# Performance work log

Hardware: AMD Instinct MI355X
Metric: run time of the kernel (lower is better)

Reference implementation:

```python
import jax, jax.numpy as jnp
import numpy as np

IMG = 100          # IMG_SIZE
NQ = 4             # N_QUBITS
STEP = 2           # sqrt(NQ)
NP_SIDE = IMG // STEP   # 50 patches per side
NPATCH = NP_SIDE * NP_SIDE  # 2500

# Fixed surrogate for tq.RandomLayer(n_ops=8): 6 param rotations + 2 CNOTs
OPS = [("rx", 0), ("ry", 1), ("rz", 2), ("cnot", (0, 1)),
       ("rx", 3), ("cnot", (2, 3)), ("ry", 0), ("rz", 1)]


def _apply_1q(psi, G, w):
    # psi: [N,2,2,2,2] complex, G: [2,2] complex, wire w
    out = jnp.tensordot(G, psi, axes=[[1], [w + 1]])  # new wire axis at 0
    return jnp.moveaxis(out, 0, w + 1)


def _apply_cnot(psi, c, t):
    p0 = jax.lax.index_in_dim(psi, 0, axis=c + 1, keepdims=True)
    p1 = jax.lax.index_in_dim(psi, 1, axis=c + 1, keepdims=True)
    p1 = jnp.flip(p1, axis=t + 1)  # X on target when control=1
    return jnp.concatenate([p0, p1], axis=c + 1)


def _gate(name, t):
    tc = t.astype(jnp.complex64)
    c, s = jnp.cos(tc / 2), jnp.sin(tc / 2)
    if name == "rx":
        return jnp.stack([jnp.stack([c, -1j * s]), jnp.stack([-1j * s, c])])
    if name == "ry":
        return jnp.stack([jnp.stack([c, -s]), jnp.stack([s, c])])
    # rz
    em, ep = jnp.exp(-0.5j * tc), jnp.exp(0.5j * tc)
    z = jnp.zeros_like(em)
    return jnp.stack([jnp.stack([em, z]), jnp.stack([z, ep])])


def _quanv(x, q_params):
    # x: [B,100,100] -> batched 4-qubit statevector sim over all patches
    B = x.shape[0]
    # patch pixel order: [x[c,r], x[c,r+1], x[c+1,r], x[c+1,r+1]]
    p = x.reshape(B, NP_SIDE, STEP, NP_SIDE, STEP)
    p = p.transpose(0, 1, 3, 2, 4).reshape(B * NPATCH, NQ)  # [N,4] angles
    half = 0.5 * p
    a = jnp.stack([jnp.cos(half), jnp.sin(half)], axis=-1)  # [N,4,2] RY|0>
    psi = jnp.einsum("na,nb,nc,nd->nabcd", a[:, 0], a[:, 1], a[:, 2], a[:, 3])
    psi = psi.astype(jnp.complex64)
    pi = 0
    for name, w in OPS:
        if name == "cnot":
            psi = _apply_cnot(psi, w[0], w[1])
        else:
            psi = _apply_1q(psi, _gate(name, q_params[pi]), w)
            pi += 1
    probs = jnp.abs(psi) ** 2  # [N,2,2,2,2] real
    zsign = jnp.array([1.0, -1.0], dtype=probs.dtype)
    exps = []
    for w in range(NQ):
        zb = zsign.reshape((1,) + (1,) * w + (2,) + (1,) * (NQ - 1 - w))
        exps.append((probs * zb).sum(axis=(1, 2, 3, 4)))
    meas = jnp.stack(exps, axis=-1)  # [N,4] PauliZ expvals
    return meas.reshape(B, NPATCH * NQ).astype(jnp.float32)  # [B,10000]


def setup_inputs() -> dict:
    key = jax.random.key(0)
    k1, k2, k3, k4 = jax.random.split(key, 4)
    x = jax.random.uniform(k1, (64, IMG, IMG), dtype=jnp.float32)
    W = jax.random.normal(k2, (2, IMG * IMG), dtype=jnp.float32) * 0.01
    b = jax.random.normal(k3, (2,), dtype=jnp.float32) * 0.01
    q_params = jax.random.uniform(k4, (6,), dtype=jnp.float32) * 2.0 * np.pi
    return {"x": x, "W": W, "b": b, "q_params": q_params}


def reference(x, W, b, q_params):
    feats = jax.lax.stop_gradient(_quanv(x, q_params))  # torch.no_grad() block
    logits = feats @ W.T + b
    return jax.nn.log_softmax(logits, axis=-1)
```

## Files before the change

### kernel.cpp

```cpp
#include <hip/hip_runtime.h>
#include <math.h>

#define IMG      100
#define NPS      50
#define NPATCH   2500
#define NIMG     64
#define BLK      1024


__global__ __launch_bounds__(BLK) void quanv_fused_kernel(
    const float* __restrict__ x,
    const float* __restrict__ W,
    const float* __restrict__ bias,
    const float* __restrict__ qp,
    float* __restrict__ out)
{
    const int b = blockIdx.x;

    const float C0 = __cosf(qp[0]);
    float S1, C1;  __sincosf(qp[1], &S1, &C1);
    const float C3 = __cosf(qp[3]);
    float S4, C4;  __sincosf(qp[4], &S4, &C4);

    const float k_a = C0 * C4;
    const float k_b = S4 * C1;
    const float k_c = S4 * S1;
    const float k_d = C0 * C1;
    const float k_e = C0 * S1;
    const float k_f = C3;

    float t0 = 0.0f, t1 = 0.0f;

    const float* xb = x + b * (IMG * IMG);

    for (int p = threadIdx.x; p < NPATCH; p += BLK) {
        const int pi = p / NPS;
        const int pj = p - pi * NPS;

        const float2 r0 = *reinterpret_cast<const float2*>(xb + (2 * pi) * IMG + 2 * pj);
        const float2 r1 = *reinterpret_cast<const float2*>(xb + (2 * pi + 1) * IMG + 2 * pj);
        const float x0 = r0.x, x1 = r0.y, x2 = r1.x, x3 = r1.y;

        float sx0, cz0, sx1, cz1;
        __sincosf(x0, &sx0, &cz0);
        __sincosf(x1, &sx1, &cz1);
        const float cz2 = __cosf(x2);
        const float cz3 = __cosf(x3);

        const float e0 = k_a * cz0 - k_b * sx0 * sx1 - k_c * sx0 * cz1;
        const float e1 = k_d * cz0 * cz1 - k_e * cz0 * sx1;
        const float e2 = cz2;
        const float e3 = k_f * cz2 * cz3;

        const float4 w0 = reinterpret_cast<const float4*>(W)[p];
        const float4 w1 = reinterpret_cast<const float4*>(W)[NPATCH + p];
        t0 += e0 * w0.x + e1 * w0.y + e2 * w0.z + e3 * w0.w;
        t1 += e0 * w1.x + e1 * w1.y + e2 * w1.z + e3 * w1.w;
    }

    #pragma unroll
    for (int off = 32; off > 0; off >>= 1) {
        t0 += __shfl_down(t0, off);
        t1 += __shfl_down(t1, off);
    }
    __shared__ float red0[BLK / 64], red1[BLK / 64];
    const int lane = threadIdx.x & 63;
    const int wv   = threadIdx.x >> 6;
    if (lane == 0) { red0[wv] = t0; red1[wv] = t1; }
    __syncthreads();
    if (threadIdx.x == 0) {
        float l0 = 0.f, l1 = 0.f;
        #pragma unroll
        for (int w = 0; w < BLK / 64; ++w) { l0 += red0[w]; l1 += red1[w]; }
        l0 += bias[0];
        l1 += bias[1];
        float m   = fmaxf(l0, l1);
        float lse = m + logf(__expf(l0 - m) + __expf(l1 - m));
        out[b * 2 + 0] = l0 - lse;
        out[b * 2 + 1] = l1 - lse;
    }
}

extern "C" void kernel_launch(void* const* d_in, const int* in_sizes, int n_in,
                              void* d_out, int out_size, void* d_ws, size_t ws_size,
                              hipStream_t stream) {
    const float* x    = (const float*)d_in[0];
    const float* W    = (const float*)d_in[1];
    const float* bias = (const float*)d_in[2];
    const float* qp   = (const float*)d_in[3];
    float* out = (float*)d_out;

    quanv_fused_kernel<<<NIMG, BLK, 0, stream>>>(x, W, bias, qp, out);
}
```

Before: 61.26 us.

## Split each image across four blocks with a separate finalize kernel

Each image's patch range is split into four slices, so 256 blocks of 256 threads run instead of 64 blocks of 1024. This spreads the work over more compute units on a GPU with many CUs. Per-slice partial logits go to workspace, and a second small kernel adds bias and computes the log-softmax. The cost is an extra kernel launch and a round trip through global memory.

```diff
diff --git a/kernel.cpp b/kernel.cpp
--- a/kernel.cpp
+++ b/kernel.cpp
@@ -5,17 +5,20 @@
 #define NPS      50
 #define NPATCH   2500
 #define NIMG     64
-#define BLK      1024
+#define NSLICE   4
+#define SLPATCH  (NPATCH / NSLICE)
+#define BLK1     256
 
 
-__global__ __launch_bounds__(BLK) void quanv_fused_kernel(
+__global__ __launch_bounds__(BLK1) void quanv_part_kernel(
     const float* __restrict__ x,
     const float* __restrict__ W,
-    const float* __restrict__ bias,
     const float* __restrict__ qp,
-    float* __restrict__ out)
+    float2* __restrict__ partial)
 {
-    const int b = blockIdx.x;
+    const int blk = blockIdx.x;
+    const int b   = blk >> 2;
+    const int s   = blk & 3;
 
     const float C0 = __cosf(qp[0]);
     float S1, C1;  __sincosf(qp[1], &S1, &C1);
@@ -32,20 +35,20 @@
     float t0 = 0.0f, t1 = 0.0f;
 
     const float* xb = x + b * (IMG * IMG);
+    const int p_end = (s + 1) * SLPATCH;
 
-    for (int p = threadIdx.x; p < NPATCH; p += BLK) {
+    for (int p = s * SLPATCH + threadIdx.x; p < p_end; p += BLK1) {
         const int pi = p / NPS;
         const int pj = p - pi * NPS;
 
         const float2 r0 = *reinterpret_cast<const float2*>(xb + (2 * pi) * IMG + 2 * pj);
         const float2 r1 = *reinterpret_cast<const float2*>(xb + (2 * pi + 1) * IMG + 2 * pj);
-        const float x0 = r0.x, x1 = r0.y, x2 = r1.x, x3 = r1.y;
 
         float sx0, cz0, sx1, cz1;
-        __sincosf(x0, &sx0, &cz0);
-        __sincosf(x1, &sx1, &cz1);
-        const float cz2 = __cosf(x2);
-        const float cz3 = __cosf(x3);
+        __sincosf(r0.x, &sx0, &cz0);
+        __sincosf(r0.y, &sx1, &cz1);
+        const float cz2 = __cosf(r1.x);
+        const float cz3 = __cosf(r1.y);
 
         const float e0 = k_a * cz0 - k_b * sx0 * sx1 - k_c * sx0 * cz1;
         const float e1 = k_d * cz0 * cz1 - k_e * cz0 * sx1;
@@ -63,22 +66,36 @@
         t0 += __shfl_down(t0, off);
         t1 += __shfl_down(t1, off);
     }
-    __shared__ float red0[BLK / 64], red1[BLK / 64];
+    __shared__ float2 red[BLK1 / 64];
     const int lane = threadIdx.x & 63;
     const int wv   = threadIdx.x >> 6;
-    if (lane == 0) { red0[wv] = t0; red1[wv] = t1; }
+    if (lane == 0) red[wv] = make_float2(t0, t1);
     __syncthreads();
     if (threadIdx.x == 0) {
-        float l0 = 0.f, l1 = 0.f;
+        float a0 = 0.f, a1 = 0.f;
         #pragma unroll
-        for (int w = 0; w < BLK / 64; ++w) { l0 += red0[w]; l1 += red1[w]; }
-        l0 += bias[0];
-        l1 += bias[1];
-        float m   = fmaxf(l0, l1);
-        float lse = m + logf(__expf(l0 - m) + __expf(l1 - m));
-        out[b * 2 + 0] = l0 - lse;
-        out[b * 2 + 1] = l1 - lse;
+        for (int w = 0; w < BLK1 / 64; ++w) { a0 += red[w].x; a1 += red[w].y; }
+        partial[blk] = make_float2(a0, a1);
     }
+}
+
+__global__ __launch_bounds__(64) void finalize_kernel(
+    const float2* __restrict__ partial,
+    const float* __restrict__ bias,
+    float* __restrict__ out)
+{
+    const int b = threadIdx.x;
+    float l0 = bias[0], l1 = bias[1];
+    #pragma unroll
+    for (int s = 0; s < NSLICE; ++s) {
+        const float2 pr = partial[b * NSLICE + s];
+        l0 += pr.x;
+        l1 += pr.y;
+    }
+    const float m   = fmaxf(l0, l1);
+    const float lse = m + logf(__expf(l0 - m) + __expf(l1 - m));
+    out[b * 2 + 0] = l0 - lse;
+    out[b * 2 + 1] = l1 - lse;
 }
 
 extern "C" void kernel_launch(void* const* d_in, const int* in_sizes, int n_in,
@@ -90,5 +107,8 @@
     const float* qp   = (const float*)d_in[3];
     float* out = (float*)d_out;
 
-    quanv_fused_kernel<<<NIMG, BLK, 0, stream>>>(x, W, bias, qp, out);
+    float2* partial = (float2*)d_ws;
+
+    quanv_part_kernel<<<NIMG * NSLICE, BLK1, 0, stream>>>(x, W, qp, partial);
+    finalize_kernel<<<1, 64, 0, stream>>>(partial, bias, out);
 }
```

Measured after the change: 62.71 us. +2.4%, slower.
